# Performance work log

Hardware: AMD Instinct MI355X
Metric: run time of the kernel (lower is better)

The kernel has to match this reference:

```python
import jax, jax.numpy as jnp
import numpy as np

EPSILON = 0.05
SINKHORN_ITERS = 3
TEMP = 0.1
PROB_RATIO = 1.0
LAMBD = 15.0
MU = 1.0
NU = 1.0
GAMMA = 0.2

B, D, K = 16384, 512, 2048


def setup_inputs() -> dict:
    key = jax.random.key(0)
    k1, k2, k3 = jax.random.split(key, 3)
    z_1 = jax.random.normal(k1, (B, D), dtype=jnp.float32)
    z_2 = jax.random.normal(k2, (B, D), dtype=jnp.float32)
    W = jax.random.normal(k3, (K, D), dtype=jnp.float32) * (1.0 / np.sqrt(D))
    return {"z_1": z_1, "z_2": z_2, "W": W}


def _compute_v(z):
    # unbiased variance over batch dim, matching torch.var default
    var = jnp.var(z, axis=0, ddof=1)
    return jnp.mean(jnp.maximum(0.0, GAMMA - jnp.sqrt(var + 1e-8)))


def _compute_c(z):
    n, d = z.shape
    zc = z - jnp.mean(z, axis=0, keepdims=True)
    C = (zc.T @ zc) / (n - 1)  # [d, d] unbiased covariance (torch.cov)
    off = C - jnp.diag(jnp.diag(C))
    return jnp.sum(off * off) / d


def _l2norm(z):
    return z / jnp.clip(jnp.linalg.norm(z, axis=-1, keepdims=True), 1e-12)


def _sinkhorn(out):
    # out: [B, K] raw logits (no grad path)
    b, k = out.shape
    Q = jnp.exp(out / EPSILON).T  # [K, B]
    Q = Q / jnp.sum(Q)
    for _ in range(SINKHORN_ITERS):
        Q = Q / (jnp.sum(Q, axis=1, keepdims=True) * k)
        Q = Q / (jnp.sum(Q, axis=0, keepdims=True) * b)
    Q = Q * b
    return Q.T  # [B, K]


def reference(z_1, z_2, W):
    v_z1 = _compute_v(z_1)
    v_z2 = _compute_v(z_2)
    c_z1 = _compute_c(z_1)
    c_z2 = _compute_c(z_2)

    z1n = _l2norm(z_1)
    z2n = _l2norm(z_2)
    logits_1 = z1n @ W.T  # [B, K]
    logits_2 = z2n @ W.T

    tgt_w_1 = jax.lax.stop_gradient(logits_1 * PROB_RATIO + logits_2 * (1 - PROB_RATIO))
    tgt_w_2 = jax.lax.stop_gradient(logits_2 * PROB_RATIO + logits_1 * (1 - PROB_RATIO))
    tgt_probs_1 = _sinkhorn(tgt_w_1)
    tgt_probs_2 = _sinkhorn(tgt_w_2)

    l1 = logits_1 / TEMP
    l2 = logits_2 / TEMP
    lp1 = jax.nn.log_softmax(l1, axis=1)
    lp2 = jax.nn.log_softmax(l2, axis=1)

    loss_ce = -0.5 * (jnp.mean(jnp.sum(tgt_probs_1 * lp2, axis=1))
                      + jnp.mean(jnp.sum(tgt_probs_2 * lp1, axis=1)))
    loss_var = v_z1 + v_z2
    loss_cov = c_z1 + c_z2
    loss = LAMBD * loss_ce + MU * loss_var + NU * loss_cov

    # diagnostics (no-grad in original)
    logits = jnp.concatenate([l1, l2], axis=0)  # [2B, K]
    k_idx = jnp.argmax(logits, axis=-1)
    hard_probs = jnp.zeros((K,), logits.dtype).at[k_idx].add(1.0) / logits.shape[0]
    code_perplexity = jnp.exp(-jnp.sum(hard_probs * jnp.log(hard_probs + 1e-7)))
    avg_probs = jnp.mean(jax.nn.softmax(logits, axis=-1), axis=0)
    prob_perplexity = jnp.exp(-jnp.sum(avg_probs * jnp.log(avg_probs + 1e-7)))
    acc_1 = jnp.mean((jnp.argmax(l1, axis=1) == jnp.argmax(tgt_probs_2, axis=1)).astype(jnp.float32))
    acc_2 = jnp.mean((jnp.argmax(l2, axis=1) == jnp.argmax(tgt_probs_1, axis=1)).astype(jnp.float32))
    acc = 0.5 * (acc_1 + acc_2)

    return (loss, loss_ce, loss_var, loss_cov, code_perplexity, prob_perplexity, acc)
```

## Files before the change

kernel.cpp:

```cpp
#include <hip/hip_runtime.h>
#include <hip/hip_bf16.h>

#define B_N 16384
#define D_N 512
#define K_N 2048

typedef __attribute__((ext_vector_type(8))) short bf16x8;
typedef __attribute__((ext_vector_type(4))) float f32x4;
typedef __attribute__((ext_vector_type(4))) unsigned short u16x4;
typedef unsigned short u16;

__device__ __forceinline__ float bf2f(short s) {
  return __builtin_bit_cast(float, ((unsigned)(u16)s) << 16);
}
__device__ __forceinline__ u16 f2bf(float x) {
  return __builtin_bit_cast(u16, __float2bfloat16(x));
}
__device__ __forceinline__ unsigned fbits(float x) {
  return __builtin_bit_cast(unsigned, x);
}
__device__ __forceinline__ float wred_sum(float v) {
#pragma unroll
  for (int o = 32; o; o >>= 1) v += __shfl_down(v, o, 64);
  return v;
}

__device__ __forceinline__ void gld16(const u16* g, const u16* l) {
  __builtin_amdgcn_global_load_lds((const __attribute__((address_space(1))) void*)g,
                                   (__attribute__((address_space(3))) void*)l, 16, 0, 0);
}

__global__ __launch_bounds__(256) void k_rownorm(const float* __restrict__ z1,
                                                 const float* __restrict__ z2,
                                                 u16* __restrict__ zn1, u16* __restrict__ zn2,
                                                 u16* __restrict__ zb1, u16* __restrict__ zb2) {
  int wid = threadIdx.x >> 6, lane = threadIdx.x & 63;
  int row = blockIdx.x * 4 + wid;
  const float* z; u16 *zn, *zb; int r;
  if (row < B_N) { z = z1; zn = zn1; zb = zb1; r = row; }
  else { z = z2; zn = zn2; zb = zb2; r = row - B_N; }
  const float4* zr = (const float4*)(z + (size_t)r * D_N);
  float4 va = zr[lane], vb = zr[lane + 64];
  float ss = va.x*va.x + va.y*va.y + va.z*va.z + va.w*va.w
           + vb.x*vb.x + vb.y*vb.y + vb.z*vb.z + vb.w*vb.w;
#pragma unroll
  for (int o = 32; o; o >>= 1) ss += __shfl_xor(ss, o, 64);
  float inv = 1.0f / fmaxf(sqrtf(ss), 1e-12f);
  u16x4 pa = {f2bf(va.x), f2bf(va.y), f2bf(va.z), f2bf(va.w)};
  u16x4 pb = {f2bf(vb.x), f2bf(vb.y), f2bf(vb.z), f2bf(vb.w)};
  u16x4 na = {f2bf(va.x*inv), f2bf(va.y*inv), f2bf(va.z*inv), f2bf(va.w*inv)};
  u16x4 nb = {f2bf(vb.x*inv), f2bf(vb.y*inv), f2bf(vb.z*inv), f2bf(vb.w*inv)};
  ((u16x4*)(zb + (size_t)r * D_N))[lane] = pa;
  ((u16x4*)(zb + (size_t)r * D_N))[lane + 64] = pb;
  ((u16x4*)(zn + (size_t)r * D_N))[lane] = na;
  ((u16x4*)(zn + (size_t)r * D_N))[lane + 64] = nb;
}

__global__ __launch_bounds__(256) void k_convW(const float* __restrict__ W,
                                               u16* __restrict__ Wb) {
  size_t base = ((size_t)blockIdx.x * 256 + threadIdx.x) * 8;
#pragma unroll
  for (int j = 0; j < 8; j++) Wb[base + j] = f2bf(W[base + j]);
}

__global__ __launch_bounds__(512) void k_colstats(const u16* __restrict__ zb1,
                                                  const u16* __restrict__ zb2,
                                                  float* __restrict__ csum,
                                                  float* __restrict__ csumsq) {
  int zi = blockIdx.z;
  const u16* z = zi ? zb2 : zb1;
  __shared__ float s1[512], s2[512];
  int t = threadIdx.y * 64 + threadIdx.x;
  s1[t] = 0.f; s2[t] = 0.f;
  __syncthreads();
  int c0 = threadIdx.x * 8;
  float a[8], a2[8];
#pragma unroll
  for (int e = 0; e < 8; e++) { a[e] = 0.f; a2[e] = 0.f; }
  for (int u = 0; u < 16; u++) {
    int r = blockIdx.y * 128 + threadIdx.y + 8 * u;
    bf16x8 v = *(const bf16x8*)&z[(size_t)r * D_N + c0];
#pragma unroll
    for (int e = 0; e < 8; e++) { float x = bf2f(v[e]); a[e] += x; a2[e] += x * x; }
  }
#pragma unroll
  for (int e = 0; e < 8; e++) {
    atomicAdd(&s1[c0 + e], a[e]);
    atomicAdd(&s2[c0 + e], a2[e]);
  }
  __syncthreads();
  atomicAdd(&csum[zi * D_N + t], s1[t]);
  atomicAdd(&csumsq[zi * D_N + t], s2[t]);
}

__global__ __launch_bounds__(256) void k_vloss(const float* __restrict__ csum,
                                               const float* __restrict__ csumsq,
                                               float* __restrict__ scal) {
  int idx = blockIdx.x * 256 + threadIdx.x;
  float s = csum[idx], sq = csumsq[idx];
  float mean = s * (1.0f / (float)B_N);
  float var = (sq - (float)B_N * mean * mean) * (1.0f / (float)(B_N - 1));
  float term = fmaxf(0.f, 0.2f - sqrtf(var + 1e-8f));
  term = wred_sum(term);
  __shared__ float sw[4];
  if ((threadIdx.x & 63) == 0) sw[threadIdx.x >> 6] = term;
  __syncthreads();
  if (threadIdx.x == 0) atomicAdd(&scal[0], sw[0] + sw[1] + sw[2] + sw[3]);
}

__global__ __launch_bounds__(256) void k_gram(const u16* __restrict__ zb1,
                                              const u16* __restrict__ zb2,
                                              float* __restrict__ Gpart) {
  int zi = blockIdx.z >> 4, chunk = blockIdx.z & 15;
  const u16* z = zi ? zb2 : zb1;
  int ti = 0, xx = blockIdx.x;
  while (xx >= 8 - ti) { xx -= 8 - ti; ti++; }
  int tj = ti + xx;
  int i0 = ti * 64, j0 = tj * 64;
  __shared__ u16 lA[64][32], lB[64][32];
  int t = threadIdx.x, wid = t >> 6, lane = t & 63;
  int br = t & 31, fg = t >> 5;
  f32x4 acc[4];
#pragma unroll
  for (int q = 0; q < 4; q++) acc[q] = (f32x4){0.f, 0.f, 0.f, 0.f};
  for (int bb = 0; bb < 1024; bb += 32) {
    size_t rb = ((size_t)chunk * 1024 + bb + br) * D_N;
    bf16x8 va = *(const bf16x8*)&z[rb + i0 + fg * 8];
    bf16x8 vb = *(const bf16x8*)&z[rb + j0 + fg * 8];
#pragma unroll
    for (int e = 0; e < 8; e++) {
      lA[fg * 8 + e][br] = (u16)va[e];
      lB[fg * 8 + e][br] = (u16)vb[e];
    }
    __syncthreads();
    int m = lane & 15, q = lane >> 4;
    bf16x8 a = *(const bf16x8*)&lA[16 * wid + m][8 * q];
#pragma unroll
    for (int tt = 0; tt < 4; tt++) {
      bf16x8 b = *(const bf16x8*)&lB[16 * tt + m][8 * q];
      acc[tt] = __builtin_amdgcn_mfma_f32_16x16x32_bf16(a, b, acc[tt], 0, 0, 0);
    }
    __syncthreads();
  }
  float* gp = Gpart + (((size_t)zi * 16 + chunk) * 36 + blockIdx.x) * 4096;
  int n = lane & 15, q = lane >> 4;
#pragma unroll
  for (int tt = 0; tt < 4; tt++)
#pragma unroll
    for (int r = 0; r < 4; r++)
      gp[(16 * wid + q * 4 + r) * 64 + 16 * tt + n] = acc[tt][r];
}

__global__ __launch_bounds__(256) void k_covreduce(const float* __restrict__ Gpart,
                                                   const float* __restrict__ csum,
                                                   float* __restrict__ scal) {
  int zi = blockIdx.y;
  int tile = blockIdx.x >> 4, part = blockIdx.x & 15;
  int ti = 0, xx = tile;
  while (xx >= 8 - ti) { xx -= 8 - ti; ti++; }
  int tj = ti + xx;
  int idx = part * 256 + threadIdx.x;
  int li = idx >> 6, lj = idx & 63;
  int i = ti * 64 + li, j = tj * 64 + lj;
  float g = 0.f;
#pragma unroll
  for (int c = 0; c < 16; c++)
    g += Gpart[(((size_t)zi * 16 + c) * 36 + tile) * 4096 + idx];
  float mi = csum[zi * D_N + i] * (1.0f / (float)B_N);
  float mj = csum[zi * D_N + j] * (1.0f / (float)B_N);
  float C = (g - (float)B_N * mi * mj) * (1.0f / (float)(B_N - 1));
  float wgt = (ti == tj) ? ((li == lj) ? 0.f : 1.f) : 2.f;
  float v = wgt * C * C;
  v = wred_sum(v);
  __shared__ float sw[4];
  if ((threadIdx.x & 63) == 0) sw[threadIdx.x >> 6] = v;
  __syncthreads();
  if (threadIdx.x == 0) atomicAdd(&scal[1], sw[0] + sw[1] + sw[2] + sw[3]);
}

__device__ __forceinline__ bf16x8 fragld(const u16* base, int row, int ks, int lane) {
  int seg = (ks * 4 + (lane >> 4)) ^ (row & 7);
  return *(const bf16x8*)&base[row * 64 + seg * 8];
}

__device__ __forceinline__ void stage256(const u16* __restrict__ G, int grow0,
                                         int d0, const u16* ldsbase, int t) {
#pragma unroll
  for (int q = 0; q < 4; q++) {
    int row = q * 64 + (t >> 3);
    int scol = ((t & 7) ^ ((t >> 3) & 7)) * 8;
    gld16(G + (size_t)(grow0 + row) * D_N + d0 + scol,
          ldsbase + q * 4096 + (t >> 6) * 512);
  }
}

__device__ __forceinline__ void comp256(const u16* tA, const u16* tB,
                                        f32x4 (&acc)[8][4], int wm, int wn, int lane) {
  bf16x8 bq[4][2];
#pragma unroll
  for (int j = 0; j < 4; j++)
#pragma unroll
    for (int ks = 0; ks < 2; ks++)
      bq[j][ks] = fragld(tB, wn * 64 + j * 16 + (lane & 15), ks, lane);
#pragma unroll
  for (int q = 0; q < 4; q++) {
    bf16x8 aq[2][2];
#pragma unroll
    for (int i2 = 0; i2 < 2; i2++)
#pragma unroll
      for (int ks = 0; ks < 2; ks++)
        aq[i2][ks] = fragld(tA, wm * 128 + (q * 2 + i2) * 16 + (lane & 15), ks, lane);
    __builtin_amdgcn_s_setprio(1);
#pragma unroll
    for (int i2 = 0; i2 < 2; i2++)
#pragma unroll
      for (int j = 0; j < 4; j++)
#pragma unroll
        for (int ks = 0; ks < 2; ks++)
          acc[q * 2 + i2][j] = __builtin_amdgcn_mfma_f32_16x16x32_bf16(
              bq[j][ks], aq[i2][ks], acc[q * 2 + i2][j], 0, 0, 0);
    __builtin_amdgcn_s_setprio(0);
  }
}

__global__ __launch_bounds__(512, 2) void k_logits(const u16* __restrict__ zn1,
                                                   const u16* __restrict__ zn2,
                                                   const u16* __restrict__ Wb,
                                                   u16* __restrict__ L1, u16* __restrict__ L2,
                                                   float* __restrict__ rowsum) {
  __shared__ u16 lds[65536];
  int hw = blockIdx.x + 64 * (blockIdx.y + 8 * blockIdx.z);
  int l = (hw & 7) * 128 + (hw >> 3);
  int zi = l >> 9, by = (l >> 6) & 7, bx = l & 63;
  const u16* A = zi ? zn2 : zn1;
  u16* Lout = zi ? L2 : L1;
  int b0 = bx * 256, k0 = by * 256;
  int t = threadIdx.x, lane = t & 63, wid = t >> 6;
  int wm = wid >> 2, wn = wid & 3;
  f32x4 acc[8][4];
#pragma unroll
  for (int i = 0; i < 8; i++)
#pragma unroll
    for (int j = 0; j < 4; j++) acc[i][j] = (f32x4){0.f, 0.f, 0.f, 0.f};

  stage256(A, b0, 0, lds, t);
  stage256(Wb, k0, 0, lds + 16384, t);
  stage256(A, b0, 64, lds + 32768, t);
  stage256(Wb, k0, 64, lds + 49152, t);
  asm volatile("s_waitcnt vmcnt(8)\n\ts_barrier" ::: "memory");

#pragma unroll
  for (int kt = 0; kt < 8; kt++) {
    const u16* tA = lds + (kt & 1) * 32768;
    comp256(tA, tA + 16384, acc, wm, wn, lane);
    if (kt < 6) {
      asm volatile("s_barrier" ::: "memory");
      const u16* dst = lds + (kt & 1) * 32768;
      stage256(A, b0, (kt + 2) * 64, dst, t);
      stage256(Wb, k0, (kt + 2) * 64, dst + 16384, t);
      asm volatile("s_waitcnt vmcnt(8)\n\ts_barrier" ::: "memory");
    } else if (kt == 6) {
      asm volatile("s_waitcnt vmcnt(0)\n\ts_barrier" ::: "memory");
    }
  }

  __syncthreads();
  float* red = (float*)lds;
  if (t < 256) red[t] = 0.f;
  __syncthreads();
  int cb = lane & 15;
  int cq = lane >> 4;
  float rp[16];
#pragma unroll
  for (int q = 0; q < 16; q++) rp[q] = 0.f;
#pragma unroll
  for (int i = 0; i < 8; i++)
#pragma unroll
    for (int j = 0; j < 4; j++) {
      f32x4 v = acc[i][j];
      u16x4 h = {f2bf(v[0]), f2bf(v[1]), f2bf(v[2]), f2bf(v[3])};
      int gb = b0 + wm * 128 + i * 16 + cb;
      int gk = k0 + wn * 64 + j * 16 + cq * 4;
      *(u16x4*)&Lout[(size_t)gb * K_N + gk] = h;
#pragma unroll
      for (int r = 0; r < 4; r++)
        rp[j * 4 + r] += __expf(20.0f * bf2f((short)h[r]));
    }
#pragma unroll
  for (int q = 0; q < 16; q++) {
#pragma unroll
    for (int o = 1; o < 16; o <<= 1) rp[q] += __shfl_xor(rp[q], o, 64);
  }
  if (cb == 0) {
#pragma unroll
    for (int j = 0; j < 4; j++)
#pragma unroll
      for (int r = 0; r < 4; r++)
        atomicAdd(&red[wn * 64 + j * 16 + cq * 4 + r], rp[j * 4 + r]);
  }
  __syncthreads();
  if (t < 256) atomicAdd(&rowsum[(size_t)zi * 3 * K_N + k0 + t], red[t]);
}

__global__ __launch_bounds__(256) void k_sink(const u16* __restrict__ L1,
                                              const u16* __restrict__ L2,
                                              float* __restrict__ rowsum, int it) {
  int zi = blockIdx.y;
  const u16* L = zi ? L2 : L1;
  const float* rs_in = rowsum + ((size_t)zi * 3 + it) * K_N;
  float* rs_out = rowsum + ((size_t)zi * 3 + it + 1) * K_N;
  __shared__ float pm[K_N];
  int t = threadIdx.x, lane = t & 63, wid = t >> 6;
  for (int k = t; k < K_N; k += 256) pm[k] = 0.f;
  float rv[32];
#pragma unroll
  for (int jj = 0; jj < 4; jj++) {
    const float4* p = (const float4*)&rs_in[jj * 512 + lane * 8];
    float4 x = p[0], y = p[1];
    rv[jj*8+0] = 1.0f / ((float)K_N * x.x); rv[jj*8+1] = 1.0f / ((float)K_N * x.y);
    rv[jj*8+2] = 1.0f / ((float)K_N * x.z); rv[jj*8+3] = 1.0f / ((float)K_N * x.w);
    rv[jj*8+4] = 1.0f / ((float)K_N * y.x); rv[jj*8+5] = 1.0f / ((float)K_N * y.y);
    rv[jj*8+6] = 1.0f / ((float)K_N * y.z); rv[jj*8+7] = 1.0f / ((float)K_N * y.w);
  }
  __syncthreads();
  float racc[32];
#pragma unroll
  for (int q = 0; q < 32; q++) racc[q] = 0.f;
  int w = blockIdx.x * 4 + wid;
  const u16* Lw = L + (size_t)w * 8 * K_N;
  bf16x8 bufA[4], bufB[4];
#pragma unroll
  for (int jj = 0; jj < 4; jj++)
    bufA[jj] = *(const bf16x8*)&Lw[jj * 512 + lane * 8];
#pragma unroll
  for (int rr = 0; rr < 8; rr++) {
    const bf16x8* cur = (rr & 1) ? bufB : bufA;
    bf16x8* nxt = (rr & 1) ? bufA : bufB;
    if (rr < 7) {
#pragma unroll
      for (int jj = 0; jj < 4; jj++)
        nxt[jj] = *(const bf16x8*)&Lw[(rr + 1) * K_N + jj * 512 + lane * 8];
    }
    float c = 0.f;
#pragma unroll
    for (int jj = 0; jj < 4; jj++)
#pragma unroll
      for (int e = 0; e < 8; e++)
        c += __expf(20.0f * bf2f(cur[jj][e])) * rv[jj * 8 + e];
#pragma unroll
    for (int o = 32; o; o >>= 1) c += __shfl_xor(c, o, 64);
    float cb = 1.0f / ((float)B_N * c);
#pragma unroll
    for (int jj = 0; jj < 4; jj++)
#pragma unroll
      for (int e = 0; e < 8; e++)
        racc[jj * 8 + e] += __expf(20.0f * bf2f(cur[jj][e])) * cb;
  }
#pragma unroll
  for (int q = 0; q < 32; q++)
    atomicAdd(&pm[(q & 7) * 256 + (q >> 3) * 64 + lane], racc[q]);
  __syncthreads();
  for (int k = t; k < K_N; k += 256)
    atomicAdd(&rs_out[k], pm[(k & 7) * 256 + (k >> 3)]);
}

__global__ __launch_bounds__(256, 2) void k_final(const u16* __restrict__ L1,
                                                  const u16* __restrict__ L2,
                                                  const float* __restrict__ rowsum,
                                                  float* __restrict__ probsum,
                                                  int* __restrict__ counts,
                                                  float* __restrict__ scal) {
  __shared__ float pmerge[K_N];
  const float* rs1 = rowsum + 2 * K_N;
  const float* rs2 = rowsum + 5 * K_N;
  int t = threadIdx.x, lane = t & 63, wid = t >> 6;
  for (int k = t; k < K_N; k += 256) pmerge[k] = 0.f;
  float rv1[32], rv2[32];
#pragma unroll
  for (int jj = 0; jj < 4; jj++) {
    const float4* p1 = (const float4*)&rs1[jj * 512 + lane * 8];
    const float4* p2 = (const float4*)&rs2[jj * 512 + lane * 8];
    float4 x1 = p1[0], y1 = p1[1], x2 = p2[0], y2 = p2[1];
    rv1[jj*8+0] = 1.0f/((float)K_N*x1.x); rv1[jj*8+1] = 1.0f/((float)K_N*x1.y);
    rv1[jj*8+2] = 1.0f/((float)K_N*x1.z); rv1[jj*8+3] = 1.0f/((float)K_N*x1.w);
    rv1[jj*8+4] = 1.0f/((float)K_N*y1.x); rv1[jj*8+5] = 1.0f/((float)K_N*y1.y);
    rv1[jj*8+6] = 1.0f/((float)K_N*y1.z); rv1[jj*8+7] = 1.0f/((float)K_N*y1.w);
    rv2[jj*8+0] = 1.0f/((float)K_N*x2.x); rv2[jj*8+1] = 1.0f/((float)K_N*x2.y);
    rv2[jj*8+2] = 1.0f/((float)K_N*x2.z); rv2[jj*8+3] = 1.0f/((float)K_N*x2.w);
    rv2[jj*8+4] = 1.0f/((float)K_N*y2.x); rv2[jj*8+5] = 1.0f/((float)K_N*y2.y);
    rv2[jj*8+6] = 1.0f/((float)K_N*y2.z); rv2[jj*8+7] = 1.0f/((float)K_N*y2.w);
  }
  __syncthreads();
  float pacc[32];
#pragma unroll
  for (int q = 0; q < 32; q++) pacc[q] = 0.f;
  float ce_acc = 0.f; int acc_cnt = 0;
  int w = blockIdx.x * 4 + wid;
  for (int pp = 0; pp < 8; pp++) {
    int ba = w * 16 + pp * 2;
    bf16x8 va1[4], va2[4], vb1[4], vb2[4];
#pragma unroll
    for (int jj = 0; jj < 4; jj++) {
      va1[jj] = *(const bf16x8*)&L1[(size_t)ba * K_N + jj * 512 + lane * 8];
      va2[jj] = *(const bf16x8*)&L2[(size_t)ba * K_N + jj * 512 + lane * 8];
      vb1[jj] = *(const bf16x8*)&L1[(size_t)(ba + 1) * K_N + jj * 512 + lane * 8];
      vb2[jj] = *(const bf16x8*)&L2[(size_t)(ba + 1) * K_N + jj * 512 + lane * 8];
    }
    float sE1a=0,sE2a=0,d12a=0,d21a=0,Z1a=0,Z2a=0;
    float sE1b=0,sE2b=0,d12b=0,d21b=0,Z1b=0,Z2b=0;
    unsigned um1a=0,um2a=0,ua1a=0,ua2a=0;
    unsigned um1b=0,um2b=0,ua1b=0,ua2b=0;
#pragma unroll
    for (int jj = 0; jj < 4; jj++)
#pragma unroll
      for (int e = 0; e < 8; e++) {
        int q = jj * 8 + e;
        unsigned ik = 2047u - (unsigned)(jj * 512 + lane * 8 + e);
        float x1 = bf2f(va1[jj][e]), x2 = bf2f(va2[jj][e]);
        float t1 = __expf(10.0f * x1), t2 = __expf(10.0f * x2);
        float e1 = t1 * t1 * rv1[q], e2 = t2 * t2 * rv2[q];
        sE1a += e1; sE2a += e2; d12a += e1 * x2; d21a += e2 * x1; Z1a += t1; Z2a += t2;
        um1a = max(um1a, (fbits(t1) & 0xFFFFF800u) | ik);
        um2a = max(um2a, (fbits(t2) & 0xFFFFF800u) | ik);
        ua1a = max(ua1a, (fbits(e1) & 0xFFFFF800u) | ik);
        ua2a = max(ua2a, (fbits(e2) & 0xFFFFF800u) | ik);
        x1 = bf2f(vb1[jj][e]); x2 = bf2f(vb2[jj][e]);
        t1 = __expf(10.0f * x1); t2 = __expf(10.0f * x2);
        e1 = t1 * t1 * rv1[q]; e2 = t2 * t2 * rv2[q];
        sE1b += e1; sE2b += e2; d12b += e1 * x2; d21b += e2 * x1; Z1b += t1; Z2b += t2;
        um1b = max(um1b, (fbits(t1) & 0xFFFFF800u) | ik);
        um2b = max(um2b, (fbits(t2) & 0xFFFFF800u) | ik);
        ua1b = max(ua1b, (fbits(e1) & 0xFFFFF800u) | ik);
        ua2b = max(ua2b, (fbits(e2) & 0xFFFFF800u) | ik);
      }
#pragma unroll
    for (int o = 32; o; o >>= 1) {
      sE1a += __shfl_xor(sE1a, o, 64); sE2a += __shfl_xor(sE2a, o, 64);
      d12a += __shfl_xor(d12a, o, 64); d21a += __shfl_xor(d21a, o, 64);
      Z1a += __shfl_xor(Z1a, o, 64);   Z2a += __shfl_xor(Z2a, o, 64);
      sE1b += __shfl_xor(sE1b, o, 64); sE2b += __shfl_xor(sE2b, o, 64);
      d12b += __shfl_xor(d12b, o, 64); d21b += __shfl_xor(d21b, o, 64);
      Z1b += __shfl_xor(Z1b, o, 64);   Z2b += __shfl_xor(Z2b, o, 64);
      um1a = max(um1a, (unsigned)__shfl_xor((int)um1a, o, 64));
      um2a = max(um2a, (unsigned)__shfl_xor((int)um2a, o, 64));
      ua1a = max(ua1a, (unsigned)__shfl_xor((int)ua1a, o, 64));
      ua2a = max(ua2a, (unsigned)__shfl_xor((int)ua2a, o, 64));
      um1b = max(um1b, (unsigned)__shfl_xor((int)um1b, o, 64));
      um2b = max(um2b, (unsigned)__shfl_xor((int)um2b, o, 64));
      ua1b = max(ua1b, (unsigned)__shfl_xor((int)ua1b, o, 64));
      ua2b = max(ua2b, (unsigned)__shfl_xor((int)ua2b, o, 64));
    }
    {
      int m1i = 2047 - (int)(um1a & 2047u), m2i = 2047 - (int)(um2a & 2047u);
      int a1i = 2047 - (int)(ua1a & 2047u), a2i = 2047 - (int)(ua2a & 2047u);
      float invc1 = 1.0f / sE1a, invc2 = 1.0f / sE2a;
      ce_acc += (10.0f * d12a) * invc1 - __logf(Z2a) + (10.0f * d21a) * invc2 - __logf(Z1a);
      acc_cnt += (m1i == a2i) + (m2i == a1i);
      if (lane == 0) { atomicAdd(&counts[m1i], 1); atomicAdd(&counts[m2i], 1); }
      float iZ1 = 1.0f / Z1a, iZ2 = 1.0f / Z2a;
#pragma unroll
      for (int jj = 0; jj < 4; jj++)
#pragma unroll
        for (int e = 0; e < 8; e++)
          pacc[jj * 8 + e] += __expf(10.0f * bf2f(va1[jj][e])) * iZ1
                            + __expf(10.0f * bf2f(va2[jj][e])) * iZ2;
    }
    {
      int m1i = 2047 - (int)(um1b & 2047u), m2i = 2047 - (int)(um2b & 2047u);
      int a1i = 2047 - (int)(ua1b & 2047u), a2i = 2047 - (int)(ua2b & 2047u);
      float invc1 = 1.0f / sE1b, invc2 = 1.0f / sE2b;
      ce_acc += (10.0f * d12b) * invc1 - __logf(Z2b) + (10.0f * d21b) * invc2 - __logf(Z1b);
      acc_cnt += (m1i == a2i) + (m2i == a1i);
      if (lane == 0) { atomicAdd(&counts[m1i], 1); atomicAdd(&counts[m2i], 1); }
      float iZ1 = 1.0f / Z1b, iZ2 = 1.0f / Z2b;
#pragma unroll
      for (int jj = 0; jj < 4; jj++)
#pragma unroll
        for (int e = 0; e < 8; e++)
          pacc[jj * 8 + e] += __expf(10.0f * bf2f(vb1[jj][e])) * iZ1
                            + __expf(10.0f * bf2f(vb2[jj][e])) * iZ2;
    }
  }
  if (lane == 0) {
    atomicAdd(&scal[2], ce_acc);
    atomicAdd(&scal[3], (float)acc_cnt);
  }
#pragma unroll
  for (int q = 0; q < 32; q++)
    atomicAdd(&pmerge[(q & 7) * 256 + (q >> 3) * 64 + lane], pacc[q]);
  __syncthreads();
  for (int k = t; k < K_N; k += 256) atomicAdd(&probsum[k], pmerge[k]);
}

__global__ __launch_bounds__(256) void k_combine(const float* __restrict__ scal,
                                                 const float* __restrict__ probsum,
                                                 const int* __restrict__ counts,
                                                 float* __restrict__ out) {
  int t = threadIdx.x;
  float ec = 0.f, ep = 0.f;
  for (int k = t; k < K_N; k += 256) {
    float p = (float)counts[k] * (1.0f / (2.0f * (float)B_N));
    ec += -p * __logf(p + 1e-7f);
    float q = probsum[k] * (1.0f / (2.0f * (float)B_N));
    ep += -q * __logf(q + 1e-7f);
  }
  ec = wred_sum(ec);
  ep = wred_sum(ep);
  __shared__ float se[4], sp[4];
  if ((t & 63) == 0) { se[t >> 6] = ec; sp[t >> 6] = ep; }
  __syncthreads();
  if (t == 0) {
    float tec = se[0] + se[1] + se[2] + se[3];
    float tep = sp[0] + sp[1] + sp[2] + sp[3];
    float ce = -0.5f * scal[2] * (1.0f / (float)B_N);
    float lvar = scal[0] * (1.0f / (float)D_N);
    float lcov = scal[1] * (1.0f / (float)D_N);
    float acc = scal[3] * (1.0f / (2.0f * (float)B_N));
    out[0] = 15.0f * ce + lvar + lcov;
    out[1] = ce;
    out[2] = lvar;
    out[3] = lcov;
    out[4] = __expf(tec);
    out[5] = __expf(tep);
    out[6] = acc;
  }
}

extern "C" void kernel_launch(void* const* d_in, const int* in_sizes, int n_in,
                              void* d_out, int out_size, void* d_ws, size_t ws_size,
                              hipStream_t stream) {
  (void)in_sizes; (void)n_in; (void)out_size; (void)ws_size;
  const float* z1 = (const float*)d_in[0];
  const float* z2 = (const float*)d_in[1];
  const float* W = (const float*)d_in[2];

  char* w = (char*)d_ws;
  size_t off = 0;
  auto take = [&](size_t b) -> void* {
    void* p = w + off;
    off = (off + b + 255) & ~(size_t)255;
    return p;
  };
  float* rowsum = (float*)take(2 * 3 * K_N * 4);
  float* csum = (float*)take(2 * D_N * 4);
  float* csumsq = (float*)take(2 * D_N * 4);
  float* probsum = (float*)take(K_N * 4);
  int* counts = (int*)take(K_N * 4);
  float* scal = (float*)take(64);
  size_t zero_bytes = off;
  u16* zn1 = (u16*)take((size_t)B_N * D_N * 2);
  u16* zn2 = (u16*)take((size_t)B_N * D_N * 2);
  u16* Wb = (u16*)take((size_t)K_N * D_N * 2);
  u16* L1 = (u16*)take((size_t)B_N * K_N * 2);
  u16* L2 = (u16*)take((size_t)B_N * K_N * 2);
  float* Gpart = (float*)take((size_t)2 * 16 * 36 * 4096 * 4);
  u16* zb1 = L1;
  u16* zb2 = L1 + (size_t)B_N * D_N;

  hipMemsetAsync(d_ws, 0, zero_bytes, stream);

  k_rownorm<<<8192, 256, 0, stream>>>(z1, z2, zn1, zn2, zb1, zb2);
  k_convW<<<512, 256, 0, stream>>>(W, Wb);
  k_colstats<<<dim3(1, 128, 2), dim3(64, 8), 0, stream>>>(zb1, zb2, csum, csumsq);
  k_vloss<<<4, 256, 0, stream>>>(csum, csumsq, scal);
  k_gram<<<dim3(36, 1, 32), 256, 0, stream>>>(zb1, zb2, Gpart);
  k_covreduce<<<dim3(36 * 16, 2), 256, 0, stream>>>(Gpart, csum, scal);
  k_logits<<<dim3(64, 8, 2), 512, 0, stream>>>(zn1, zn2, Wb, L1, L2, rowsum);
  k_sink<<<dim3(512, 2), 256, 0, stream>>>(L1, L2, rowsum, 0);
  k_sink<<<dim3(512, 2), 256, 0, stream>>>(L1, L2, rowsum, 1);
  k_final<<<256, 256, 0, stream>>>(L1, L2, rowsum, probsum, counts, scal);
  k_combine<<<1, 256, 0, stream>>>(scal, probsum, counts, (float*)d_out);
}
```

Measured before the change: 544.8 us.

## Split each k_final row across two wavefronts and quadruple grid size

k_final now assigns each pair of rows to two wavefronts, each covering half of the K columns. Partial sums and argmax keys are exchanged through shared memory with two block barriers per iteration, and the grid grows from 256 to 1024 blocks. This halves per-thread register arrays, drops the two-blocks-per-SM launch bound, and raises parallelism and latency hiding for the memory-bound final pass. The cost is the extra barriers and shared-memory exchange on every row pair, plus more atomics into the global probsum array.

```diff
diff --git a/kernel.cpp b/kernel.cpp
--- a/kernel.cpp
+++ b/kernel.cpp
@@ -364,22 +364,25 @@
     atomicAdd(&rs_out[k], pm[(k & 7) * 256 + (k >> 3)]);
 }
 
-__global__ __launch_bounds__(256, 2) void k_final(const u16* __restrict__ L1,
-                                                  const u16* __restrict__ L2,
-                                                  const float* __restrict__ rowsum,
-                                                  float* __restrict__ probsum,
-                                                  int* __restrict__ counts,
-                                                  float* __restrict__ scal) {
+__global__ __launch_bounds__(256) void k_final(const u16* __restrict__ L1,
+                                               const u16* __restrict__ L2,
+                                               const float* __restrict__ rowsum,
+                                               float* __restrict__ probsum,
+                                               int* __restrict__ counts,
+                                               float* __restrict__ scal) {
   __shared__ float pmerge[K_N];
+  __shared__ float xw[4][20];
   const float* rs1 = rowsum + 2 * K_N;
   const float* rs2 = rowsum + 5 * K_N;
   int t = threadIdx.x, lane = t & 63, wid = t >> 6;
+  int half = wid & 1;
+  int tl = half * 64 + lane;
   for (int k = t; k < K_N; k += 256) pmerge[k] = 0.f;
-  float rv1[32], rv2[32];
-#pragma unroll
-  for (int jj = 0; jj < 4; jj++) {
-    const float4* p1 = (const float4*)&rs1[jj * 512 + lane * 8];
-    const float4* p2 = (const float4*)&rs2[jj * 512 + lane * 8];
+  float rv1[16], rv2[16];
+#pragma unroll
+  for (int jj = 0; jj < 2; jj++) {
+    const float4* p1 = (const float4*)&rs1[jj * 1024 + tl * 8];
+    const float4* p2 = (const float4*)&rs2[jj * 1024 + tl * 8];
     float4 x1 = p1[0], y1 = p1[1], x2 = p2[0], y2 = p2[1];
     rv1[jj*8+0] = 1.0f/((float)K_N*x1.x); rv1[jj*8+1] = 1.0f/((float)K_N*x1.y);
     rv1[jj*8+2] = 1.0f/((float)K_N*x1.z); rv1[jj*8+3] = 1.0f/((float)K_N*x1.w);
@@ -391,31 +394,31 @@
     rv2[jj*8+6] = 1.0f/((float)K_N*y2.z); rv2[jj*8+7] = 1.0f/((float)K_N*y2.w);
   }
   __syncthreads();
-  float pacc[32];
-#pragma unroll
-  for (int q = 0; q < 32; q++) pacc[q] = 0.f;
+  float pacc[16];
+#pragma unroll
+  for (int q = 0; q < 16; q++) pacc[q] = 0.f;
   float ce_acc = 0.f; int acc_cnt = 0;
-  int w = blockIdx.x * 4 + wid;
-  for (int pp = 0; pp < 8; pp++) {
-    int ba = w * 16 + pp * 2;
-    bf16x8 va1[4], va2[4], vb1[4], vb2[4];
-#pragma unroll
-    for (int jj = 0; jj < 4; jj++) {
-      va1[jj] = *(const bf16x8*)&L1[(size_t)ba * K_N + jj * 512 + lane * 8];
-      va2[jj] = *(const bf16x8*)&L2[(size_t)ba * K_N + jj * 512 + lane * 8];
-      vb1[jj] = *(const bf16x8*)&L1[(size_t)(ba + 1) * K_N + jj * 512 + lane * 8];
-      vb2[jj] = *(const bf16x8*)&L2[(size_t)(ba + 1) * K_N + jj * 512 + lane * 8];
+  int w = blockIdx.x * 2 + (wid >> 1);
+  for (int pp = 0; pp < 4; pp++) {
+    int ba = w * 8 + pp * 2;
+    bf16x8 va1[2], va2[2], vb1[2], vb2[2];
+#pragma unroll
+    for (int jj = 0; jj < 2; jj++) {
+      va1[jj] = *(const bf16x8*)&L1[(size_t)ba * K_N + jj * 1024 + tl * 8];
+      va2[jj] = *(const bf16x8*)&L2[(size_t)ba * K_N + jj * 1024 + tl * 8];
+      vb1[jj] = *(const bf16x8*)&L1[(size_t)(ba + 1) * K_N + jj * 1024 + tl * 8];
+      vb2[jj] = *(const bf16x8*)&L2[(size_t)(ba + 1) * K_N + jj * 1024 + tl * 8];
     }
     float sE1a=0,sE2a=0,d12a=0,d21a=0,Z1a=0,Z2a=0;
     float sE1b=0,sE2b=0,d12b=0,d21b=0,Z1b=0,Z2b=0;
     unsigned um1a=0,um2a=0,ua1a=0,ua2a=0;
     unsigned um1b=0,um2b=0,ua1b=0,ua2b=0;
 #pragma unroll
-    for (int jj = 0; jj < 4; jj++)
+    for (int jj = 0; jj < 2; jj++)
 #pragma unroll
       for (int e = 0; e < 8; e++) {
         int q = jj * 8 + e;
-        unsigned ik = 2047u - (unsigned)(jj * 512 + lane * 8 + e);
+        unsigned ik = 2047u - (unsigned)(jj * 1024 + tl * 8 + e);
         float x1 = bf2f(va1[jj][e]), x2 = bf2f(va2[jj][e]);
         float t1 = __expf(10.0f * x1), t2 = __expf(10.0f * x2);
         float e1 = t1 * t1 * rv1[q], e2 = t2 * t2 * rv2[q];
@@ -450,16 +453,34 @@
       ua1b = max(ua1b, (unsigned)__shfl_xor((int)ua1b, o, 64));
       ua2b = max(ua2b, (unsigned)__shfl_xor((int)ua2b, o, 64));
     }
+    if (lane == 0) {
+      float* xp = xw[wid];
+      xp[0]=sE1a; xp[1]=sE2a; xp[2]=d12a; xp[3]=d21a; xp[4]=Z1a; xp[5]=Z2a;
+      xp[6]=sE1b; xp[7]=sE2b; xp[8]=d12b; xp[9]=d21b; xp[10]=Z1b; xp[11]=Z2b;
+      unsigned* xu = (unsigned*)(xp + 12);
+      xu[0]=um1a; xu[1]=um2a; xu[2]=ua1a; xu[3]=ua2a;
+      xu[4]=um1b; xu[5]=um2b; xu[6]=ua1b; xu[7]=ua2b;
+    }
+    __syncthreads();
+    {
+      const float* xp = xw[wid ^ 1];
+      sE1a+=xp[0]; sE2a+=xp[1]; d12a+=xp[2]; d21a+=xp[3]; Z1a+=xp[4]; Z2a+=xp[5];
+      sE1b+=xp[6]; sE2b+=xp[7]; d12b+=xp[8]; d21b+=xp[9]; Z1b+=xp[10]; Z2b+=xp[11];
+      const unsigned* xu = (const unsigned*)(xp + 12);
+      um1a=max(um1a,xu[0]); um2a=max(um2a,xu[1]); ua1a=max(ua1a,xu[2]); ua2a=max(ua2a,xu[3]);
+      um1b=max(um1b,xu[4]); um2b=max(um2b,xu[5]); ua1b=max(ua1b,xu[6]); ua2b=max(ua2b,xu[7]);
+    }
+    __syncthreads();
     {
       int m1i = 2047 - (int)(um1a & 2047u), m2i = 2047 - (int)(um2a & 2047u);
       int a1i = 2047 - (int)(ua1a & 2047u), a2i = 2047 - (int)(ua2a & 2047u);
       float invc1 = 1.0f / sE1a, invc2 = 1.0f / sE2a;
       ce_acc += (10.0f * d12a) * invc1 - __logf(Z2a) + (10.0f * d21a) * invc2 - __logf(Z1a);
       acc_cnt += (m1i == a2i) + (m2i == a1i);
-      if (lane == 0) { atomicAdd(&counts[m1i], 1); atomicAdd(&counts[m2i], 1); }
+      if (lane == 0 && half == 0) { atomicAdd(&counts[m1i], 1); atomicAdd(&counts[m2i], 1); }
       float iZ1 = 1.0f / Z1a, iZ2 = 1.0f / Z2a;
 #pragma unroll
-      for (int jj = 0; jj < 4; jj++)
+      for (int jj = 0; jj < 2; jj++)
 #pragma unroll
         for (int e = 0; e < 8; e++)
           pacc[jj * 8 + e] += __expf(10.0f * bf2f(va1[jj][e])) * iZ1
@@ -471,23 +492,25 @@
       float invc1 = 1.0f / sE1b, invc2 = 1.0f / sE2b;
       ce_acc += (10.0f * d12b) * invc1 - __logf(Z2b) + (10.0f * d21b) * invc2 - __logf(Z1b);
       acc_cnt += (m1i == a2i) + (m2i == a1i);
-      if (lane == 0) { atomicAdd(&counts[m1i], 1); atomicAdd(&counts[m2i], 1); }
+      if (lane == 0 && half == 0) { atomicAdd(&counts[m1i], 1); atomicAdd(&counts[m2i], 1); }
       float iZ1 = 1.0f / Z1b, iZ2 = 1.0f / Z2b;
 #pragma unroll
-      for (int jj = 0; jj < 4; jj++)
+      for (int jj = 0; jj < 2; jj++)
 #pragma unroll
         for (int e = 0; e < 8; e++)
           pacc[jj * 8 + e] += __expf(10.0f * bf2f(vb1[jj][e])) * iZ1
                             + __expf(10.0f * bf2f(vb2[jj][e])) * iZ2;
     }
   }
-  if (lane == 0) {
+  if (lane == 0 && half == 0) {
     atomicAdd(&scal[2], ce_acc);
     atomicAdd(&scal[3], (float)acc_cnt);
   }
 #pragma unroll
-  for (int q = 0; q < 32; q++)
-    atomicAdd(&pmerge[(q & 7) * 256 + (q >> 3) * 64 + lane], pacc[q]);
+  for (int jj = 0; jj < 2; jj++)
+#pragma unroll
+    for (int e = 0; e < 8; e++)
+      atomicAdd(&pmerge[e * 256 + jj * 128 + tl], pacc[jj * 8 + e]);
   __syncthreads();
   for (int k = t; k < K_N; k += 256) atomicAdd(&probsum[k], pmerge[k]);
 }
@@ -568,6 +591,6 @@
   k_logits<<<dim3(64, 8, 2), 512, 0, stream>>>(zn1, zn2, Wb, L1, L2, rowsum);
   k_sink<<<dim3(512, 2), 256, 0, stream>>>(L1, L2, rowsum, 0);
   k_sink<<<dim3(512, 2), 256, 0, stream>>>(L1, L2, rowsum, 1);
-  k_final<<<256, 256, 0, stream>>>(L1, L2, rowsum, probsum, counts, scal);
+  k_final<<<1024, 256, 0, stream>>>(L1, L2, rowsum, probsum, counts, scal);
   k_combine<<<1, 256, 0, stream>>>(scal, probsum, counts, (float*)d_out);
 }
```

Result: faster. 515.9 us (-5.3%).
